# Performance work log

Measured on AMD Instinct MI355X. Metric: run time of the kernel, lower is better.

Reference implementation:

```python
import jax, jax.numpy as jnp
import numpy as np
import math

B, S, HID, H = 2, 1024, 768, 12
D = HID // H  # 64
ALPHA = 32.0


def setup_inputs() -> dict:
    key = jax.random.key(0)
    ks = jax.random.split(key, 8)
    return {
        "hidden_states": jax.random.normal(ks[0], (B, S, HID), jnp.float32),
        "attention_mask": jnp.zeros((B, 1, 1, S), jnp.float32),
        "head_mask": jnp.ones((1, H, 1, 1), jnp.float32),
        "rel_pos": jax.random.normal(ks[1], (B, H, S, S), jnp.float32),
        "rel_2d_pos": jax.random.normal(ks[2], (B, H, S, S), jnp.float32),
        "Wq": jax.random.normal(ks[3], (HID, HID), jnp.float32) * 0.02,
        "bq": jnp.zeros((HID,), jnp.float32),
        "Wk": jax.random.normal(ks[4], (HID, HID), jnp.float32) * 0.02,
        "bk": jnp.zeros((HID,), jnp.float32),
        "Wv": jax.random.normal(ks[5], (HID, HID), jnp.float32) * 0.02,
        "bv": jnp.zeros((HID,), jnp.float32),
    }


def _heads(x):
    # [B,S,HID] -> [B,H,S,D]
    return x.reshape(B, S, H, D).transpose(0, 2, 1, 3)


def cogview_softmax(scores, alpha=ALPHA):
    s = scores / alpha
    m = jnp.max(s, axis=-1, keepdims=True)
    return jax.nn.softmax((s - m) * alpha, axis=-1)


def reference(hidden_states, attention_mask, head_mask, rel_pos, rel_2d_pos,
              Wq, bq, Wk, bk, Wv, bv):
    norm = math.sqrt(D)
    q = _heads(hidden_states @ Wq + bq) / norm   # [B,H,S,D]
    k = _heads(hidden_states @ Wk + bk)
    v = _heads(hidden_states @ Wv + bv)
    scores = jnp.einsum("bhsd,bhtd->bhst", q, k)
    scores = scores + (rel_pos + rel_2d_pos) / norm
    scores = scores + attention_mask
    probs = cogview_softmax(scores)              # [B,H,S,S]
    probs = probs * head_mask
    ctx = jnp.einsum("bhst,bhtd->bhsd", probs, v)
    ctx = ctx.transpose(0, 2, 1, 3).reshape(B, S, HID)
    return ctx
```

## Files before the change

### kernel.cpp

```cpp
#include <hip/hip_runtime.h>
#include <hip/hip_bf16.h>
#include <cstdint>

#define BB   2
#define SS   1024
#define HIDD 768
#define NH   12
#define DH   64
#define BH   (BB*NH)

typedef short bf16x8 __attribute__((ext_vector_type(8)));
typedef float f32x4  __attribute__((ext_vector_type(4)));

__device__ __forceinline__ unsigned short f2b(float x) {
    union { float f; uint32_t u; } v; v.f = x;
    uint32_t u = v.u;
    uint32_t r = (u + 0x7fffu + ((u >> 16) & 1u)) >> 16;
    return (unsigned short)r;
}

__device__ __forceinline__ void async16(const void* g, void* l) {
    __builtin_amdgcn_global_load_lds(
        (const __attribute__((address_space(1))) unsigned int*)g,
        (__attribute__((address_space(3))) unsigned int*)l,
        16, 0, 0);
}

__global__ void cvt_x(const float* __restrict__ x, unsigned short* __restrict__ xb) {
    int i = blockIdx.x * blockDim.x + threadIdx.x;
    float4 v = ((const float4*)x)[i];
    ushort4 o;
    o.x = f2b(v.x); o.y = f2b(v.y); o.z = f2b(v.z); o.w = f2b(v.w);
    ((ushort4*)xb)[i] = o;
}

__global__ void transpose_w(const float* __restrict__ Wq, const float* __restrict__ Wk,
                            const float* __restrict__ Wv, unsigned short* __restrict__ Wt) {
    __shared__ float tile[32][33];
    const int w = blockIdx.z;
    const float* W = (w == 0) ? Wq : (w == 1) ? Wk : Wv;
    const int tx = threadIdx.x & 31, ty = threadIdx.x >> 5;
    const int k0 = blockIdx.x * 32, n0 = blockIdx.y * 32;
    for (int p = 0; p < 4; ++p)
        tile[ty + p * 8][tx] = W[(k0 + ty + p * 8) * HIDD + n0 + tx];
    __syncthreads();
    for (int p = 0; p < 4; ++p) {
        int n = n0 + ty + p * 8;
        Wt[(w * HIDD + n) * HIDD + k0 + tx] = f2b(tile[tx][ty + p * 8]);
    }
}

__global__ __launch_bounds__(256) void qkv_gemm(
    const unsigned short* __restrict__ Xb, const unsigned short* __restrict__ Wt,
    const float* __restrict__ bq, const float* __restrict__ bk, const float* __restrict__ bv,
    unsigned short* __restrict__ Qh, unsigned short* __restrict__ Kh,
    unsigned short* __restrict__ Vh) {
    __shared__ __align__(16) unsigned short lA[2][128 * 32];
    __shared__ __align__(16) unsigned short lB[2][64 * 32];
    const int t = threadIdx.x;
    const int wave = t >> 6, lane = t & 63;
    const int l15 = lane & 15, quad = lane >> 4;
    const int m0 = blockIdx.x * 128;
    const int n0 = blockIdx.y * 64;
    const int wm = wave * 32;

    f32x4 acc[2][4] = {};

    auto stage = [&](int k0, int b) {
        #pragma unroll
        for (int r = 0; r < 2; ++r) {
            int ci = r * 256 + t;
            async16(Xb + (m0 + (ci >> 2)) * HIDD + k0 + (ci & 3) * 8,
                    &lA[b][(r * 256 + wave * 64) * 8]);
        }
        async16(Wt + (n0 + (t >> 2)) * HIDD + k0 + (t & 3) * 8,
                &lB[b][(wave * 64) * 8]);
    };

    stage(0, 0);
    for (int ki = 0; ki < 24; ++ki) {
        const int cur = ki & 1;
        __syncthreads();
        if (ki < 23) stage((ki + 1) * 32, cur ^ 1);
        bf16x8 af[2], bf[4];
        #pragma unroll
        for (int i = 0; i < 2; ++i)
            af[i] = *(const bf16x8*)&lA[cur][(wm + i * 16 + l15) * 32 + quad * 8];
        #pragma unroll
        for (int j = 0; j < 4; ++j)
            bf[j] = *(const bf16x8*)&lB[cur][(j * 16 + l15) * 32 + quad * 8];
        #pragma unroll
        for (int i = 0; i < 2; ++i)
            #pragma unroll
            for (int j = 0; j < 4; ++j)
                acc[i][j] = __builtin_amdgcn_mfma_f32_16x16x32_bf16(af[i], bf[j], acc[i][j], 0, 0, 0);
    }

    const int sect = (n0 >= 1536) ? 2 : (n0 >= 768) ? 1 : 0;
    const float* bias = (sect == 0) ? bq : (sect == 1) ? bk : bv;
    unsigned short* dst = (sect == 0) ? Qh : (sect == 1) ? Kh : Vh;
    const float scale = (sect == 0) ? 0.125f : 1.0f;
    #pragma unroll
    for (int i = 0; i < 2; ++i) {
        #pragma unroll
        for (int j = 0; j < 4; ++j) {
            int n  = n0 + j * 16 + l15;
            int nn = n - sect * HIDD;
            int h = nn >> 6, d = nn & 63;
            float bval = bias[nn];
            #pragma unroll
            for (int r = 0; r < 4; ++r) {
                int m = m0 + wm + i * 16 + quad * 4 + r;
                int b = m >> 10, s = m & 1023;
                float v = (acc[i][j][r] + bval) * scale;
                dst[((size_t)(b * NH + h) * SS + s) * DH + d] = f2b(v);
            }
        }
    }
}

__global__ __launch_bounds__(256) void transpose_v(
    const unsigned short* __restrict__ Vh, unsigned short* __restrict__ VhT) {
    __shared__ unsigned short tile[64][65];
    const int t = threadIdx.x;
    const int bh = blockIdx.y;
    const int s0 = blockIdx.x * 64;
    const int tx = t & 63, ty = t >> 6;
    const unsigned short* src = Vh + (size_t)bh * SS * DH;
    #pragma unroll
    for (int p = 0; p < 16; ++p)
        tile[ty + p * 4][tx] = src[(size_t)(s0 + ty + p * 4) * DH + tx];
    __syncthreads();
    unsigned short* dst = VhT + (size_t)bh * DH * SS;
    #pragma unroll
    for (int p = 0; p < 16; ++p)
        dst[(size_t)(ty + p * 4) * SS + s0 + tx] = tile[tx][ty + p * 4];
}

__global__ __launch_bounds__(256) void flash_attn(
    const unsigned short* __restrict__ Qh, const unsigned short* __restrict__ Kh,
    const unsigned short* __restrict__ VhT,
    const float* __restrict__ rel, const float* __restrict__ rel2d,
    const float* __restrict__ amask, const float* __restrict__ hmask,
    float* __restrict__ out) {
    __shared__ __align__(16) unsigned short Plds[4][16 * 72];
    __shared__ __align__(16) float smem[5376];

    const int t = threadIdx.x;
    const int wave = t >> 6, lane = t & 63;
    const int l15 = lane & 15, quad = lane >> 4;
    const int bh = blockIdx.y;
    const int b = bh / NH, h = bh % NH;
    const int m0 = blockIdx.x * 16;

    const unsigned short* Qp = Qh + (size_t)bh * SS * DH;
    const unsigned short* Kp = Kh + (size_t)bh * SS * DH;
    const unsigned short* Vp = VhT + (size_t)bh * DH * SS;
    const float* relp  = rel   + (size_t)bh * SS * SS;
    const float* rel2p = rel2d + (size_t)bh * SS * SS;
    const float* maskp = amask + (size_t)b * SS;

    bf16x8 qf0 = *(const bf16x8*)&Qp[(m0 + l15) * DH + quad * 8];
    bf16x8 qf1 = *(const bf16x8*)&Qp[(m0 + l15) * DH + 32 + quad * 8];

    f32x4 o[4] = {};
    float mrow[4] = {-1e30f, -1e30f, -1e30f, -1e30f};
    float lrow[4] = {0.f, 0.f, 0.f, 0.f};
    unsigned short* Pw = &Plds[wave][0];
    float* stg = &smem[wave * 1344];

    const int jbeg = wave * 256, jend = jbeg + 256;
    for (int j0 = jbeg; j0 < jend; j0 += 64) {
        f32x4 ra[4], rb[4];
        #pragma unroll
        for (int i = 0; i < 4; ++i) {
            size_t base = (size_t)(m0 + 4 * i + quad) * SS + j0 + 4 * l15;
            ra[i] = *(const f32x4*)&relp[base];
            rb[i] = *(const f32x4*)&rel2p[base];
        }
        f32x4 mk4 = *(const f32x4*)&maskp[j0 + 4 * l15];

        f32x4 sc[4] = {};
        #pragma unroll
        for (int c = 0; c < 4; ++c) {
            bf16x8 k0f = *(const bf16x8*)&Kp[(j0 + c * 16 + l15) * DH + quad * 8];
            bf16x8 k1f = *(const bf16x8*)&Kp[(j0 + c * 16 + l15) * DH + 32 + quad * 8];
            sc[c] = __builtin_amdgcn_mfma_f32_16x16x32_bf16(qf0, k0f, sc[c], 0, 0, 0);
            sc[c] = __builtin_amdgcn_mfma_f32_16x16x32_bf16(qf1, k1f, sc[c], 0, 0, 0);
        }

        #pragma unroll
        for (int i = 0; i < 4; ++i)
            #pragma unroll
            for (int cc = 0; cc < 4; ++cc)
                stg[(4 * l15 + cc) * 21 + 4 * i + quad] =
                    (ra[i][cc] + rb[i][cc]) * 0.125f + mk4[cc];

        float sv[4][4];
        #pragma unroll
        for (int c = 0; c < 4; ++c)
            #pragma unroll
            for (int r = 0; r < 4; ++r)
                sv[c][r] = sc[c][r] + stg[(c * 16 + l15) * 21 + quad * 4 + r];

        float alpha[4];
        #pragma unroll
        for (int r = 0; r < 4; ++r) {
            float mx = fmaxf(fmaxf(sv[0][r], sv[1][r]), fmaxf(sv[2][r], sv[3][r]));
            #pragma unroll
            for (int off = 1; off < 16; off <<= 1) mx = fmaxf(mx, __shfl_xor(mx, off, 64));
            float mnew = fmaxf(mrow[r], mx);
            alpha[r] = __expf(mrow[r] - mnew);
            mrow[r] = mnew;
            float rs = 0.f;
            #pragma unroll
            for (int c = 0; c < 4; ++c) {
                float p = __expf(sv[c][r] - mnew);
                sv[c][r] = p;
                rs += p;
            }
            #pragma unroll
            for (int off = 1; off < 16; off <<= 1) rs += __shfl_xor(rs, off, 64);
            lrow[r] = lrow[r] * alpha[r] + rs;
            o[0][r] *= alpha[r]; o[1][r] *= alpha[r]; o[2][r] *= alpha[r]; o[3][r] *= alpha[r];
        }
        #pragma unroll
        for (int c = 0; c < 4; ++c)
            #pragma unroll
            for (int r = 0; r < 4; ++r)
                Pw[(quad * 4 + r) * 72 + c * 16 + l15] = f2b(sv[c][r]);

        bf16x8 pf0 = *(const bf16x8*)&Pw[l15 * 72 + quad * 8];
        bf16x8 pf1 = *(const bf16x8*)&Pw[l15 * 72 + 32 + quad * 8];
        #pragma unroll
        for (int dt = 0; dt < 4; ++dt) {
            bf16x8 v0 = *(const bf16x8*)&Vp[(dt * 16 + l15) * SS + j0 + quad * 8];
            bf16x8 v1 = *(const bf16x8*)&Vp[(dt * 16 + l15) * SS + j0 + 32 + quad * 8];
            o[dt] = __builtin_amdgcn_mfma_f32_16x16x32_bf16(pf0, v0, o[dt], 0, 0, 0);
            o[dt] = __builtin_amdgcn_mfma_f32_16x16x32_bf16(pf1, v1, o[dt], 0, 0, 0);
        }
    }

    __syncthreads();
    float* o_l = smem;
    float* m_l = smem + 4096;
    float* l_l = smem + 4160;
    #pragma unroll
    for (int dt = 0; dt < 4; ++dt)
        #pragma unroll
        for (int r = 0; r < 4; ++r)
            o_l[(wave * 16 + quad * 4 + r) * 64 + dt * 16 + l15] = o[dt][r];
    if (l15 == 0) {
        #pragma unroll
        for (int r = 0; r < 4; ++r) {
            m_l[wave * 16 + quad * 4 + r] = mrow[r];
            l_l[wave * 16 + quad * 4 + r] = lrow[r];
        }
    }
    __syncthreads();

    const float hm = hmask[h];
    const int col = t & 63, rsel = t >> 6;
    #pragma unroll
    for (int rr = 0; rr < 4; ++rr) {
        int row = rsel * 4 + rr;
        float m01 = fmaxf(m_l[row], m_l[16 + row]);
        float m23 = fmaxf(m_l[32 + row], m_l[48 + row]);
        float mt = fmaxf(m01, m23);
        float lt = 0.f, val = 0.f;
        #pragma unroll
        for (int w = 0; w < 4; ++w) {
            float sc = __expf(m_l[w * 16 + row] - mt);
            lt += sc * l_l[w * 16 + row];
            val += sc * o_l[(w * 16 + row) * 64 + col];
        }
        int s = m0 + row;
        out[((size_t)(b * SS + s)) * HIDD + h * DH + col] = val * hm / lt;
    }
}

extern "C" void kernel_launch(void* const* d_in, const int* in_sizes, int n_in,
                              void* d_out, int out_size, void* d_ws, size_t ws_size,
                              hipStream_t stream) {
    const float* hs    = (const float*)d_in[0];
    const float* am    = (const float*)d_in[1];
    const float* hm    = (const float*)d_in[2];
    const float* rel   = (const float*)d_in[3];
    const float* rel2d = (const float*)d_in[4];
    const float* Wq    = (const float*)d_in[5];
    const float* bq    = (const float*)d_in[6];
    const float* Wk    = (const float*)d_in[7];
    const float* bk    = (const float*)d_in[8];
    const float* Wv    = (const float*)d_in[9];
    const float* bv    = (const float*)d_in[10];
    float* out = (float*)d_out;

    unsigned short* Xb  = (unsigned short*)d_ws;
    unsigned short* Wt  = Xb + 2048 * HIDD;
    unsigned short* Qh  = Wt + 3 * HIDD * HIDD;
    unsigned short* Kh  = Qh + (size_t)BH * SS * DH;
    unsigned short* Vh  = Kh + (size_t)BH * SS * DH;
    unsigned short* VhT = Vh + (size_t)BH * SS * DH;

    cvt_x<<<(2048 * HIDD / 4) / 256, 256, 0, stream>>>(hs, Xb);
    dim3 gT(24, 24, 3);
    transpose_w<<<gT, 256, 0, stream>>>(Wq, Wk, Wv, Wt);
    dim3 gG(16, 36);
    qkv_gemm<<<gG, 256, 0, stream>>>(Xb, Wt, bq, bk, bv, Qh, Kh, Vh);
    dim3 gV(16, BH);
    transpose_v<<<gV, 256, 0, stream>>>(Vh, VhT);
    dim3 gF(64, BH);
    flash_attn<<<gF, 256, 0, stream>>>(Qh, Kh, VhT, rel, rel2d, am, hm, out);
}
```

Measured before the change: 288.2 us.

## Prefetch bias and K tiles, drop LDS bias staging, unroll key loop

Bias values are now read directly in the MFMA accumulator layout as scalar loads, which removes the LDS staging round-trip used to transpose them. The next tile's rel/rel2d and K fragments are software-prefetched during softmax, and V fragments are loaded at the start of each iteration. The mask is preloaded into registers, shared memory is merged into one aliased buffer, and launch bounds request 2 blocks per CU. In exchange, the scalar 4-byte bias loads are less coalesced than the old 16-byte vector loads, and register pressure goes up.

```diff
diff --git a/kernel.cpp b/kernel.cpp
--- a/kernel.cpp
+++ b/kernel.cpp
@@ -137,14 +137,16 @@
         dst[(size_t)(ty + p * 4) * SS + s0 + tx] = tile[tx][ty + p * 4];
 }
 
-__global__ __launch_bounds__(256) void flash_attn(
+__global__ __launch_bounds__(256, 2) void flash_attn(
     const unsigned short* __restrict__ Qh, const unsigned short* __restrict__ Kh,
     const unsigned short* __restrict__ VhT,
     const float* __restrict__ rel, const float* __restrict__ rel2d,
     const float* __restrict__ amask, const float* __restrict__ hmask,
     float* __restrict__ out) {
-    __shared__ __align__(16) unsigned short Plds[4][16 * 72];
-    __shared__ __align__(16) float smem[5376];
+    __shared__ __align__(16) char smemraw[17408];
+    float* o_l = (float*)smemraw;
+    float* m_l = (float*)(smemraw + 16384);
+    float* l_l = (float*)(smemraw + 16640);
 
     const int t = threadIdx.x;
     const int wave = t >> 6, lane = t & 63;
@@ -160,49 +162,70 @@
     const float* rel2p = rel2d + (size_t)bh * SS * SS;
     const float* maskp = amask + (size_t)b * SS;
 
+    unsigned short* Pw = (unsigned short*)smemraw + wave * (16 * 72);
+
+    const int jbeg = wave * 256;
+
     bf16x8 qf0 = *(const bf16x8*)&Qp[(m0 + l15) * DH + quad * 8];
     bf16x8 qf1 = *(const bf16x8*)&Qp[(m0 + l15) * DH + 32 + quad * 8];
+
+    float mk_all[16];
+    #pragma unroll
+    for (int tc = 0; tc < 16; ++tc)
+        mk_all[tc] = maskp[jbeg + (tc >> 2) * 64 + (tc & 3) * 16 + l15];
 
     f32x4 o[4] = {};
     float mrow[4] = {-1e30f, -1e30f, -1e30f, -1e30f};
     float lrow[4] = {0.f, 0.f, 0.f, 0.f};
-    unsigned short* Pw = &Plds[wave][0];
-    float* stg = &smem[wave * 1344];
-
-    const int jbeg = wave * 256, jend = jbeg + 256;
-    for (int j0 = jbeg; j0 < jend; j0 += 64) {
-        f32x4 ra[4], rb[4];
-        #pragma unroll
-        for (int i = 0; i < 4; ++i) {
-            size_t base = (size_t)(m0 + 4 * i + quad) * SS + j0 + 4 * l15;
-            ra[i] = *(const f32x4*)&relp[base];
-            rb[i] = *(const f32x4*)&rel2p[base];
-        }
-        f32x4 mk4 = *(const f32x4*)&maskp[j0 + 4 * l15];
-
+
+    float ra[16], rb[16];
+    bf16x8 k0f[4], k1f[4];
+
+    #define LOAD_BIAS(J0)                                                      \
+        _Pragma("unroll")                                                      \
+        for (int c = 0; c < 4; ++c)                                            \
+            _Pragma("unroll")                                                  \
+            for (int r = 0; r < 4; ++r) {                                      \
+                size_t idx = (size_t)(m0 + quad * 4 + r) * SS + (J0) + c * 16 + l15; \
+                ra[c * 4 + r] = relp[idx];                                     \
+                rb[c * 4 + r] = rel2p[idx];                                    \
+            }
+    #define LOAD_K(J0)                                                         \
+        _Pragma("unroll")                                                      \
+        for (int c = 0; c < 4; ++c) {                                          \
+            k0f[c] = *(const bf16x8*)&Kp[((J0) + c * 16 + l15) * DH + quad * 8];      \
+            k1f[c] = *(const bf16x8*)&Kp[((J0) + c * 16 + l15) * DH + 32 + quad * 8]; \
+        }
+
+    LOAD_BIAS(jbeg)
+    LOAD_K(jbeg)
+
+    #pragma unroll
+    for (int tt = 0; tt < 4; ++tt) {
+        const int j0 = jbeg + tt * 64;
+        bf16x8 v0f[4], v1f[4];
+        #pragma unroll
+        for (int dt = 0; dt < 4; ++dt) {
+            v0f[dt] = *(const bf16x8*)&Vp[(dt * 16 + l15) * SS + j0 + quad * 8];
+            v1f[dt] = *(const bf16x8*)&Vp[(dt * 16 + l15) * SS + j0 + 32 + quad * 8];
+        }
         f32x4 sc[4] = {};
         #pragma unroll
         for (int c = 0; c < 4; ++c) {
-            bf16x8 k0f = *(const bf16x8*)&Kp[(j0 + c * 16 + l15) * DH + quad * 8];
-            bf16x8 k1f = *(const bf16x8*)&Kp[(j0 + c * 16 + l15) * DH + 32 + quad * 8];
-            sc[c] = __builtin_amdgcn_mfma_f32_16x16x32_bf16(qf0, k0f, sc[c], 0, 0, 0);
-            sc[c] = __builtin_amdgcn_mfma_f32_16x16x32_bf16(qf1, k1f, sc[c], 0, 0, 0);
-        }
-
-        #pragma unroll
-        for (int i = 0; i < 4; ++i)
-            #pragma unroll
-            for (int cc = 0; cc < 4; ++cc)
-                stg[(4 * l15 + cc) * 21 + 4 * i + quad] =
-                    (ra[i][cc] + rb[i][cc]) * 0.125f + mk4[cc];
-
+            sc[c] = __builtin_amdgcn_mfma_f32_16x16x32_bf16(qf0, k0f[c], sc[c], 0, 0, 0);
+            sc[c] = __builtin_amdgcn_mfma_f32_16x16x32_bf16(qf1, k1f[c], sc[c], 0, 0, 0);
+        }
         float sv[4][4];
         #pragma unroll
         for (int c = 0; c < 4; ++c)
             #pragma unroll
             for (int r = 0; r < 4; ++r)
-                sv[c][r] = sc[c][r] + stg[(c * 16 + l15) * 21 + quad * 4 + r];
-
+                sv[c][r] = sc[c][r] + (ra[c * 4 + r] + rb[c * 4 + r]) * 0.125f
+                         + mk_all[tt * 4 + c];
+        if (tt < 3) {
+            LOAD_BIAS(j0 + 64)
+            LOAD_K(j0 + 64)
+        }
         float alpha[4];
         #pragma unroll
         for (int r = 0; r < 4; ++r) {
@@ -234,17 +257,14 @@
         bf16x8 pf1 = *(const bf16x8*)&Pw[l15 * 72 + 32 + quad * 8];
         #pragma unroll
         for (int dt = 0; dt < 4; ++dt) {
-            bf16x8 v0 = *(const bf16x8*)&Vp[(dt * 16 + l15) * SS + j0 + quad * 8];
-            bf16x8 v1 = *(const bf16x8*)&Vp[(dt * 16 + l15) * SS + j0 + 32 + quad * 8];
-            o[dt] = __builtin_amdgcn_mfma_f32_16x16x32_bf16(pf0, v0, o[dt], 0, 0, 0);
-            o[dt] = __builtin_amdgcn_mfma_f32_16x16x32_bf16(pf1, v1, o[dt], 0, 0, 0);
-        }
-    }
+            o[dt] = __builtin_amdgcn_mfma_f32_16x16x32_bf16(pf0, v0f[dt], o[dt], 0, 0, 0);
+            o[dt] = __builtin_amdgcn_mfma_f32_16x16x32_bf16(pf1, v1f[dt], o[dt], 0, 0, 0);
+        }
+    }
+    #undef LOAD_BIAS
+    #undef LOAD_K
 
     __syncthreads();
-    float* o_l = smem;
-    float* m_l = smem + 4096;
-    float* l_l = smem + 4160;
     #pragma unroll
     for (int dt = 0; dt < 4; ++dt)
         #pragma unroll
```

Result: slower. 296.6 us (+2.9%).

## Restructure flash attention with LDS-staged double-buffered K/V and async bias loads

Applied to the files above, without the earlier changes.

Changes the attention kernel's work split. Each block now has two waves, and each wave owns 16 query rows and walks the full key range, instead of four waves splitting the key range for the same 16 rows. This removes the cross-wave softmax merge and its final LDS reduction. K and V tiles are shared across the waves through swizzled LDS, double-buffered with async global-to-LDS loads. The rel/rel2d bias tiles are also loaded asynchronously into LDS and waited on with an explicit vmcnt. The cost is a large LDS footprint (about 53 KB per block), which limits occupancy, plus a per-tile block barrier.

```diff
diff --git a/kernel.cpp b/kernel.cpp
--- a/kernel.cpp
+++ b/kernel.cpp
@@ -137,21 +137,21 @@
         dst[(size_t)(ty + p * 4) * SS + s0 + tx] = tile[tx][ty + p * 4];
 }
 
-__global__ __launch_bounds__(256) void flash_attn(
+__global__ __launch_bounds__(128) void flash_attn(
     const unsigned short* __restrict__ Qh, const unsigned short* __restrict__ Kh,
     const unsigned short* __restrict__ VhT,
     const float* __restrict__ rel, const float* __restrict__ rel2d,
     const float* __restrict__ amask, const float* __restrict__ hmask,
     float* __restrict__ out) {
-    __shared__ __align__(16) unsigned short Plds[4][16 * 72];
-    __shared__ __align__(16) float smem[5376];
+    __shared__ __align__(16) char smemraw[53760];
 
     const int t = threadIdx.x;
     const int wave = t >> 6, lane = t & 63;
     const int l15 = lane & 15, quad = lane >> 4;
+    const int l7 = l15 & 7;
     const int bh = blockIdx.y;
     const int b = bh / NH, h = bh % NH;
-    const int m0 = blockIdx.x * 16;
+    const int m0w = blockIdx.x * 32 + wave * 16;
 
     const unsigned short* Qp = Qh + (size_t)bh * SS * DH;
     const unsigned short* Kp = Kh + (size_t)bh * SS * DH;
@@ -160,48 +160,78 @@
     const float* rel2p = rel2d + (size_t)bh * SS * SS;
     const float* maskp = amask + (size_t)b * SS;
 
-    bf16x8 qf0 = *(const bf16x8*)&Qp[(m0 + l15) * DH + quad * 8];
-    bf16x8 qf1 = *(const bf16x8*)&Qp[(m0 + l15) * DH + 32 + quad * 8];
+    float* stgA = (float*)(smemraw + 32768 + wave * 8192);
+    float* stgB = stgA + 1024;
+    unsigned short* Pw = (unsigned short*)(smemraw + 49152) + wave * (16 * 72);
+
+    auto stage_kv = [&](int j0, int buf) {
+        unsigned short* dK = (unsigned short*)(smemraw + buf * 8192);
+        unsigned short* dV = (unsigned short*)(smemraw + 16384 + buf * 8192);
+        #pragma unroll
+        for (int i = 0; i < 4; ++i) {
+            int ci = i * 128 + t;
+            int row = ci >> 3, sc = ci & 7;
+            int g = sc ^ (row & 7);
+            async16(Kp + (size_t)(j0 + row) * DH + g * 8,
+                    dK + (i * 128 + wave * 64) * 8);
+            async16(Vp + (size_t)row * SS + j0 + g * 8,
+                    dV + (i * 128 + wave * 64) * 8);
+        }
+    };
+
+    auto stage_bias = [&](int j0) {
+        #pragma unroll
+        for (int i = 0; i < 4; ++i) {
+            async16(relp  + (size_t)(m0w + 4 * i + quad) * SS + j0 + l15 * 4,
+                    (char*)stgA + i * 1024);
+            async16(rel2p + (size_t)(m0w + 4 * i + quad) * SS + j0 + l15 * 4,
+                    (char*)stgB + i * 1024);
+        }
+    };
+
+    bf16x8 qf0 = *(const bf16x8*)&Qp[(m0w + l15) * DH + quad * 8];
+    bf16x8 qf1 = *(const bf16x8*)&Qp[(m0w + l15) * DH + 32 + quad * 8];
 
     f32x4 o[4] = {};
     float mrow[4] = {-1e30f, -1e30f, -1e30f, -1e30f};
     float lrow[4] = {0.f, 0.f, 0.f, 0.f};
-    unsigned short* Pw = &Plds[wave][0];
-    float* stg = &smem[wave * 1344];
-
-    const int jbeg = wave * 256, jend = jbeg + 256;
-    for (int j0 = jbeg; j0 < jend; j0 += 64) {
-        f32x4 ra[4], rb[4];
-        #pragma unroll
-        for (int i = 0; i < 4; ++i) {
-            size_t base = (size_t)(m0 + 4 * i + quad) * SS + j0 + 4 * l15;
-            ra[i] = *(const f32x4*)&relp[base];
-            rb[i] = *(const f32x4*)&rel2p[base];
-        }
-        f32x4 mk4 = *(const f32x4*)&maskp[j0 + 4 * l15];
-
-        f32x4 sc[4] = {};
+
+    stage_kv(0, 0);
+    __syncthreads();
+
+    for (int tt = 0; tt < 16; ++tt) {
+        const int j0 = tt * 64, cur = tt & 1;
+        const unsigned short* cK = (const unsigned short*)(smemraw + cur * 8192);
+        const unsigned short* cV = (const unsigned short*)(smemraw + 16384 + cur * 8192);
+
+        stage_bias(j0);
+        if (tt < 15) stage_kv(j0 + 64, cur ^ 1);
+
+        float mk[4];
+        #pragma unroll
+        for (int c = 0; c < 4; ++c) mk[c] = maskp[j0 + c * 16 + l15];
+
+        f32x4 sc4[4] = {};
         #pragma unroll
         for (int c = 0; c < 4; ++c) {
-            bf16x8 k0f = *(const bf16x8*)&Kp[(j0 + c * 16 + l15) * DH + quad * 8];
-            bf16x8 k1f = *(const bf16x8*)&Kp[(j0 + c * 16 + l15) * DH + 32 + quad * 8];
-            sc[c] = __builtin_amdgcn_mfma_f32_16x16x32_bf16(qf0, k0f, sc[c], 0, 0, 0);
-            sc[c] = __builtin_amdgcn_mfma_f32_16x16x32_bf16(qf1, k1f, sc[c], 0, 0, 0);
-        }
-
-        #pragma unroll
-        for (int i = 0; i < 4; ++i)
-            #pragma unroll
-            for (int cc = 0; cc < 4; ++cc)
-                stg[(4 * l15 + cc) * 21 + 4 * i + quad] =
-                    (ra[i][cc] + rb[i][cc]) * 0.125f + mk4[cc];
+            int row = c * 16 + l15;
+            bf16x8 k0f = *(const bf16x8*)&cK[row * 64 + (quad ^ l7) * 8];
+            bf16x8 k1f = *(const bf16x8*)&cK[row * 64 + ((quad + 4) ^ l7) * 8];
+            sc4[c] = __builtin_amdgcn_mfma_f32_16x16x32_bf16(qf0, k0f, sc4[c], 0, 0, 0);
+            sc4[c] = __builtin_amdgcn_mfma_f32_16x16x32_bf16(qf1, k1f, sc4[c], 0, 0, 0);
+        }
+
+        if (tt < 15) { asm volatile("s_waitcnt vmcnt(8)" ::: "memory"); }
+        else         { asm volatile("s_waitcnt vmcnt(0)" ::: "memory"); }
 
         float sv[4][4];
         #pragma unroll
         for (int c = 0; c < 4; ++c)
             #pragma unroll
-            for (int r = 0; r < 4; ++r)
-                sv[c][r] = sc[c][r] + stg[(c * 16 + l15) * 21 + quad * 4 + r];
+            for (int r = 0; r < 4; ++r) {
+                int fi = (quad * 4 + r) * 64 + c * 16 + l15;
+                sv[c][r] = sc4[c][r] + (stgA[fi] + stgB[fi]) * 0.125f + mk[c];
+            }
 
         float alpha[4];
         #pragma unroll
@@ -224,6 +254,7 @@
             lrow[r] = lrow[r] * alpha[r] + rs;
             o[0][r] *= alpha[r]; o[1][r] *= alpha[r]; o[2][r] *= alpha[r]; o[3][r] *= alpha[r];
         }
+
         #pragma unroll
         for (int c = 0; c < 4; ++c)
             #pragma unroll
@@ -232,50 +263,27 @@
 
         bf16x8 pf0 = *(const bf16x8*)&Pw[l15 * 72 + quad * 8];
         bf16x8 pf1 = *(const bf16x8*)&Pw[l15 * 72 + 32 + quad * 8];
+
         #pragma unroll
         for (int dt = 0; dt < 4; ++dt) {
-            bf16x8 v0 = *(const bf16x8*)&Vp[(dt * 16 + l15) * SS + j0 + quad * 8];
-            bf16x8 v1 = *(const bf16x8*)&Vp[(dt * 16 + l15) * SS + j0 + 32 + quad * 8];
-            o[dt] = __builtin_amdgcn_mfma_f32_16x16x32_bf16(pf0, v0, o[dt], 0, 0, 0);
-            o[dt] = __builtin_amdgcn_mfma_f32_16x16x32_bf16(pf1, v1, o[dt], 0, 0, 0);
-        }
-    }
-
-    __syncthreads();
-    float* o_l = smem;
-    float* m_l = smem + 4096;
-    float* l_l = smem + 4160;
+            int row = dt * 16 + l15;
+            bf16x8 v0f = *(const bf16x8*)&cV[row * 64 + (quad ^ l7) * 8];
+            bf16x8 v1f = *(const bf16x8*)&cV[row * 64 + ((quad + 4) ^ l7) * 8];
+            o[dt] = __builtin_amdgcn_mfma_f32_16x16x32_bf16(pf0, v0f, o[dt], 0, 0, 0);
+            o[dt] = __builtin_amdgcn_mfma_f32_16x16x32_bf16(pf1, v1f, o[dt], 0, 0, 0);
+        }
+
+        __syncthreads();
+    }
+
+    const float hm = hmask[h];
     #pragma unroll
-    for (int dt = 0; dt < 4; ++dt)
-        #pragma unroll
-        for (int r = 0; r < 4; ++r)
-            o_l[(wave * 16 + quad * 4 + r) * 64 + dt * 16 + l15] = o[dt][r];
-    if (l15 == 0) {
-        #pragma unroll
-        for (int r = 0; r < 4; ++r) {
-            m_l[wave * 16 + quad * 4 + r] = mrow[r];
-            l_l[wave * 16 + quad * 4 + r] = lrow[r];
-        }
-    }
-    __syncthreads();
-
-    const float hm = hmask[h];
-    const int col = t & 63, rsel = t >> 6;
-    #pragma unroll
-    for (int rr = 0; rr < 4; ++rr) {
-        int row = rsel * 4 + rr;
-        float m01 = fmaxf(m_l[row], m_l[16 + row]);
-        float m23 = fmaxf(m_l[32 + row], m_l[48 + row]);
-        float mt = fmaxf(m01, m23);
-        float lt = 0.f, val = 0.f;
-        #pragma unroll
-        for (int w = 0; w < 4; ++w) {
-            float sc = __expf(m_l[w * 16 + row] - mt);
-            lt += sc * l_l[w * 16 + row];
-            val += sc * o_l[(w * 16 + row) * 64 + col];
-        }
-        int s = m0 + row;
-        out[((size_t)(b * SS + s)) * HIDD + h * DH + col] = val * hm / lt;
+    for (int r = 0; r < 4; ++r) {
+        float inv = hm / lrow[r];
+        int s = m0w + quad * 4 + r;
+        float* op = out + ((size_t)(b * SS + s)) * HIDD + h * DH;
+        #pragma unroll
+        for (int dt = 0; dt < 4; ++dt) op[dt * 16 + l15] = o[dt][r] * inv;
     }
 }
 
@@ -309,6 +317,6 @@
     qkv_gemm<<<gG, 256, 0, stream>>>(Xb, Wt, bq, bk, bv, Qh, Kh, Vh);
     dim3 gV(16, BH);
     transpose_v<<<gV, 256, 0, stream>>>(Vh, VhT);
-    dim3 gF(64, BH);
-    flash_attn<<<gF, 256, 0, stream>>>(Qh, Kh, VhT, rel, rel2d, am, hm, out);
-}
+    dim3 gF(32, BH);
+    flash_attn<<<gF, 128, 0, stream>>>(Qh, Kh, VhT, rel, rel2d, am, hm, out);
+}
```

After: 271.8 us. -5.7%, faster.
